# Kernel optimization log

Measured on AMD Instinct MI355X. Metric: run time of the kernel, lower is better.

Reference implementation:

```python
import jax, jax.numpy as jnp
import numpy as np

NEG = -1e30  # log-domain 'zero' (safe stand-in for -inf)


def _ctc_loss(logits, labels, label_length, logit_length):
    """Dense-label CTC loss, blank = last class, logits [B,T,C] batch-major.

    Matches tf.nn.ctc_loss(blank_index=-1, logits_time_major=False):
    per-example negative log-likelihood via the standard forward algorithm
    on the blank-extended label sequence of length S = 2L+1.
    """
    B, T, C = logits.shape
    L = labels.shape[1]
    S = 2 * L + 1
    blank = C - 1

    logp = jax.nn.log_softmax(logits, axis=-1)           # [B,T,C]
    lp_t = jnp.moveaxis(logp, 1, 0)                      # [T,B,C]

    # Extended label: blank, l1, blank, l2, ..., blank
    y_ext = jnp.full((B, S), blank, dtype=labels.dtype).at[:, 1::2].set(labels)
    s_idx = jnp.arange(S)
    # s -> s-2 skip allowed iff current symbol is a non-blank differing from s-2
    y_m2 = jnp.pad(y_ext, ((0, 0), (2, 0)), constant_values=blank)[:, :-2]
    skip = (s_idx[None, :] >= 2) & (y_ext != blank) & (y_ext != y_m2)  # [B,S]

    emit0 = jnp.take_along_axis(lp_t[0], y_ext, axis=1)  # [B,S]
    alpha0 = jnp.where(s_idx[None, :] <= 1, emit0, NEG)  # paths start at s=0 or 1

    def step(alpha, lp):
        emit = jnp.take_along_axis(lp, y_ext, axis=1)                      # [B,S]
        a1 = jnp.pad(alpha, ((0, 0), (1, 0)), constant_values=NEG)[:, :-1]  # s-1
        a2 = jnp.pad(alpha, ((0, 0), (2, 0)), constant_values=NEG)[:, :-2]  # s-2
        a2 = jnp.where(skip, a2, NEG)
        new = jnp.logaddexp(jnp.logaddexp(alpha, a1), a2) + emit
        return new, new

    _, alphas = jax.lax.scan(step, alpha0, lp_t[1:])     # [T-1,B,S]
    alphas = jnp.concatenate([alpha0[None], alphas], axis=0)  # [T,B,S]

    b = jnp.arange(B)
    final = alphas[logit_length - 1, b]                  # [B,S] alpha at last frame
    end = 2 * label_length                               # index of final blank
    nll = -jnp.logaddexp(final[b, end], final[b, end - 1])
    return jnp.mean(nll)


def setup_inputs() -> dict:
    key = jax.random.key(0)
    k1, k2, k3 = jax.random.split(key, 3)
    B, T, C, L = 256, 256, 512, 64
    logits = jax.random.normal(k1, (B, T, C), dtype=jnp.float32)
    labels = jax.random.randint(k2, (B, L), 0, C - 1, dtype=jnp.int32)  # never blank
    label_length = jax.random.randint(k3, (B,), 16, L + 1, dtype=jnp.int32)
    logit_length = jnp.full((B,), T, dtype=jnp.int32)
    return {"logits": logits, "labels": labels,
            "label_length": label_length, "logit_length": logit_length}


def reference(logits, labels, label_length, logit_length):
    return _ctc_loss(logits, labels, label_length, logit_length)
```

## Files before the change

kernel.cpp:

```cpp
#include <hip/hip_runtime.h>
#include <math.h>

#define NEGV -1e30f

constexpr int Bc = 256;
constexpr int Tc = 256;
constexpr int Cc = 512;
constexpr int Lc = 64;
constexpr int PW = 8;
constexpr int NGRP = Tc / PW;
constexpr float INVLN2 = 1.44269504088896340736f;
constexpr float LN2    = 0.69314718055994530942f;

__device__ __forceinline__ float la2(float a, float b) {
    float m = fmaxf(a, b);
    float d = fabsf(a - b);
    return m + __log2f(exp2f(-d) + 1.0f);
}

__device__ __forceinline__ float lse3(float a, float b, float c) {
    float m = fmaxf(fmaxf(a, b), c);
    return m + __log2f(exp2f(a - m) + exp2f(b - m) + exp2f(c - m));
}

__device__ __forceinline__ float dpp_shr1(float x, float fill) {
    int r = __builtin_amdgcn_update_dpp(__float_as_int(fill), __float_as_int(x),
                                        0x138 , 0xF, 0xF, false);
    return __int_as_float(r);
}

__device__ __forceinline__ float wave_sum_dpp(float v) {
#define DPPADD(ctrl)                                                          \
    v += __int_as_float(__builtin_amdgcn_update_dpp(                          \
        0, __float_as_int(v), (ctrl), 0xF, 0xF, true))
    DPPADD(0x111);
    DPPADD(0x112);
    DPPADD(0x114);
    DPPADD(0x118);
    DPPADD(0x142);
    DPPADD(0x143);
#undef DPPADD
    return __int_as_float(__builtin_amdgcn_readlane(__float_as_int(v), 63));
}

__global__ __launch_bounds__(576) void ctc_k(const float* __restrict__ logits,
                                             const int* __restrict__ labels,
                                             const int* __restrict__ lab_len,
                                             const int* __restrict__ log_len,
                                             float* __restrict__ nll) {
    const int b    = blockIdx.x;
    const int tid  = threadIdx.x;
    const int w    = tid >> 6;
    const int lane = tid & 63;

    __shared__ float em[Tc][66];
    __shared__ int   done[PW];

    if (tid < PW) done[tid] = 0;
    __syncthreads();

    const float* base = logits + (size_t)b * Tc * Cc;
    const int y = labels[b * Lc + lane];

    if (w < PW) {
        const float* a0r = base + (size_t)w * Cc;
        const float* a1r = base + (size_t)(w + PW) * Cc;
        float4 c0 = ((const float4*)a0r)[lane], c1 = ((const float4*)a0r)[lane + 64];
        float  cg = a0r[y];
        float4 d0 = ((const float4*)a1r)[lane], d1 = ((const float4*)a1r)[lane + 64];
        float  dg = a1r[y];

        for (int i = 0; i < NGRP; ++i) {
            float4 e0, e1; float eg;
            if (i + 2 < NGRP) {
                const float* ar = base + (size_t)(w + PW * (i + 2)) * Cc;
                e0 = ((const float4*)ar)[lane];
                e1 = ((const float4*)ar)[lane + 64];
                eg = ar[y];
            }
            float e = __expf(c0.x) + __expf(c0.y) + __expf(c0.z) + __expf(c0.w)
                    + __expf(c1.x) + __expf(c1.y) + __expf(c1.z) + __expf(c1.w);
            float lse2 = __log2f(wave_sum_dpp(e));
            const int t = w + PW * i;
            em[t][lane] = cg * INVLN2 - lse2;
            if (lane == 63)
                em[t][64] = c1.w * INVLN2 - lse2;
            __builtin_amdgcn_sched_barrier(0);
            asm volatile("s_waitcnt lgkmcnt(0)" ::: "memory");
            if (lane == 0) *(volatile int*)&done[w] = i + 1;
            __builtin_amdgcn_sched_barrier(0);
            c0 = d0; c1 = d1; cg = dg;
            d0 = e0; d1 = e1; dg = eg;
        }
    } else {
        const int  prevlab = __shfl_up(y, 1, 64);
        const bool skip    = (lane >= 1) && (y != prevlab);
        const int  llm1    = log_len[b] - 1;
        float ae = NEGV, ao = NEGV, ax = NEGV;
        float fe = NEGV, fo = NEGV, fx = NEGV;

        auto step = [&](float em_lv, float em_bv, int t) {
            float po = dpp_shr1(ao, NEGV);
            float nae = la2(ae, po) + em_bv;
            float nao = (skip ? lse3(ao, ae, po)
                              : la2(ao, ae)) + em_lv;
            float nax = la2(ax, ao) + em_bv;
            ae = nae; ao = nao; ax = nax;
            if (t == llm1) { fe = ae; fo = ao; fx = ax; }
        };

        for (int g = 0; g < NGRP; ++g) {
            for (;;) {
                int mn = 0x7fffffff;
#pragma unroll
                for (int pw = 0; pw < PW; ++pw)
                    mn = min(mn, *(volatile int*)&done[pw]);
                if (mn > g) break;
                __builtin_amdgcn_s_sleep(2);
            }
            asm volatile("" ::: "memory");

            float el[PW], eb[PW];
#pragma unroll
            for (int r = 0; r < PW; ++r) {
                el[r] = em[PW * g + r][lane];
                eb[r] = em[PW * g + r][64];
            }
            if (g == 0) {
                ae = (lane == 0) ? eb[0] : NEGV;
                ao = (lane == 0) ? el[0] : NEGV;
                ax = NEGV;
                if (llm1 == 0) { fe = ae; fo = ao; fx = ax; }
#pragma unroll
                for (int r = 1; r < PW; ++r) step(el[r], eb[r], r);
            } else {
#pragma unroll
                for (int r = 0; r < PW; ++r) step(el[r], eb[r], PW * g + r);
            }
        }

        const int L  = lab_len[b];
        float f0 = (L == Lc) ? __shfl(fx, 63, 64) : __shfl(fe, L, 64);
        float f1 = __shfl(fo, L - 1, 64);
        if (lane == 0) nll[b] = -LN2 * la2(f0, f1);
    }
}

__global__ __launch_bounds__(256) void reduce_k(const float* __restrict__ nll,
                                                float* __restrict__ out) {
    int tid = threadIdx.x;
    float v = nll[tid];
#pragma unroll
    for (int o = 32; o; o >>= 1) v += __shfl_xor(v, o, 64);
    __shared__ float pr[4];
    if ((tid & 63) == 0) pr[tid >> 6] = v;
    __syncthreads();
    if (tid == 0) out[0] = (pr[0] + pr[1] + pr[2] + pr[3]) * (1.0f / Bc);
}

extern "C" void kernel_launch(void* const* d_in, const int* in_sizes, int n_in,
                              void* d_out, int out_size, void* d_ws, size_t ws_size,
                              hipStream_t stream) {
    const float* logits  = (const float*)d_in[0];
    const int*   labels  = (const int*)d_in[1];
    const int*   lab_len = (const int*)d_in[2];
    const int*   log_len = (const int*)d_in[3];
    float* out = (float*)d_out;
    float* nll = (float*)d_ws;

    hipLaunchKernelGGL(ctc_k, dim3(Bc), dim3(576), 0, stream,
                       logits, labels, lab_len, log_len, nll);
    hipLaunchKernelGGL(reduce_k, dim3(1), dim3(256), 0, stream, nll, out);
}
```

Baseline: 207.0 us.

## Serialize emission and recursion phases, stage rows in LDS for label gather

Removes the dedicated recursion wave and its flag-based spin-wait handoff. All 8 waves first compute log-softmax emissions for all timesteps, with a deeper 3-row prefetch. Each row is staged in shared memory so the label gather is an LDS read rather than a scattered global load. After a block barrier, wave 0 alone runs the alpha recursion. This drops the polling and extra global gathers, but the serial recursion no longer overlaps the memory-bound emission phase, and it adds 16KB of LDS per block.

```diff
diff --git a/kernel.cpp b/kernel.cpp
--- a/kernel.cpp
+++ b/kernel.cpp
@@ -8,6 +8,7 @@
 constexpr int Cc = 512;
 constexpr int Lc = 64;
 constexpr int PW = 8;
+constexpr int NROW = Tc / PW;
 constexpr int NGRP = Tc / PW;
 constexpr float INVLN2 = 1.44269504088896340736f;
 constexpr float LN2    = 0.69314718055994530942f;
@@ -43,7 +44,7 @@
     return __int_as_float(__builtin_amdgcn_readlane(__float_as_int(v), 63));
 }
 
-__global__ __launch_bounds__(576) void ctc_k(const float* __restrict__ logits,
+__global__ __launch_bounds__(512) void ctc_k(const float* __restrict__ logits,
                                              const int* __restrict__ labels,
                                              const int* __restrict__ lab_len,
                                              const int* __restrict__ log_len,
@@ -54,96 +55,85 @@
     const int lane = tid & 63;
 
     __shared__ float em[Tc][66];
-    __shared__ int   done[PW];
-
-    if (tid < PW) done[tid] = 0;
-    __syncthreads();
+    __shared__ float rows[PW][Cc];
 
     const float* base = logits + (size_t)b * Tc * Cc;
     const int y = labels[b * Lc + lane];
 
-    if (w < PW) {
-        const float* a0r = base + (size_t)w * Cc;
-        const float* a1r = base + (size_t)(w + PW) * Cc;
-        float4 c0 = ((const float4*)a0r)[lane], c1 = ((const float4*)a0r)[lane + 64];
-        float  cg = a0r[y];
-        float4 d0 = ((const float4*)a1r)[lane], d1 = ((const float4*)a1r)[lane + 64];
-        float  dg = a1r[y];
+    {
+        float* myrow = rows[w];
+        const float4* pa = (const float4*)(base + (size_t)w * Cc);
+        const float4* pb = (const float4*)(base + (size_t)(w + PW) * Cc);
+        const float4* pc = (const float4*)(base + (size_t)(w + 2 * PW) * Cc);
+        float4 a0 = pa[lane], a1 = pa[lane + 64];
+        float4 b0 = pb[lane], b1 = pb[lane + 64];
+        float4 c0 = pc[lane], c1 = pc[lane + 64];
 
-        for (int i = 0; i < NGRP; ++i) {
-            float4 e0, e1; float eg;
-            if (i + 2 < NGRP) {
-                const float* ar = base + (size_t)(w + PW * (i + 2)) * Cc;
-                e0 = ((const float4*)ar)[lane];
-                e1 = ((const float4*)ar)[lane + 64];
-                eg = ar[y];
+        for (int i = 0; i < NROW; ++i) {
+            float4 n0, n1;
+            if (i + 3 < NROW) {
+                const float4* pn =
+                    (const float4*)(base + (size_t)(w + PW * (i + 3)) * Cc);
+                n0 = pn[lane]; n1 = pn[lane + 64];
             }
-            float e = __expf(c0.x) + __expf(c0.y) + __expf(c0.z) + __expf(c0.w)
-                    + __expf(c1.x) + __expf(c1.y) + __expf(c1.z) + __expf(c1.w);
+            float e = __expf(a0.x) + __expf(a0.y) + __expf(a0.z) + __expf(a0.w)
+                    + __expf(a1.x) + __expf(a1.y) + __expf(a1.z) + __expf(a1.w);
             float lse2 = __log2f(wave_sum_dpp(e));
+            ((float4*)myrow)[lane]      = a0;
+            ((float4*)myrow)[lane + 64] = a1;
+            float xl = myrow[y];
             const int t = w + PW * i;
-            em[t][lane] = cg * INVLN2 - lse2;
+            em[t][lane] = xl * INVLN2 - lse2;
             if (lane == 63)
-                em[t][64] = c1.w * INVLN2 - lse2;
-            __builtin_amdgcn_sched_barrier(0);
-            asm volatile("s_waitcnt lgkmcnt(0)" ::: "memory");
-            if (lane == 0) *(volatile int*)&done[w] = i + 1;
-            __builtin_amdgcn_sched_barrier(0);
-            c0 = d0; c1 = d1; cg = dg;
-            d0 = e0; d1 = e1; dg = eg;
+                em[t][64] = a1.w * INVLN2 - lse2;
+            a0 = b0; a1 = b1;
+            b0 = c0; b1 = c1;
+            c0 = n0; c1 = n1;
         }
-    } else {
-        const int  prevlab = __shfl_up(y, 1, 64);
-        const bool skip    = (lane >= 1) && (y != prevlab);
-        const int  llm1    = log_len[b] - 1;
-        float ae = NEGV, ao = NEGV, ax = NEGV;
-        float fe = NEGV, fo = NEGV, fx = NEGV;
+    }
+    __syncthreads();
+    if (w != 0) return;
 
-        auto step = [&](float em_lv, float em_bv, int t) {
-            float po = dpp_shr1(ao, NEGV);
-            float nae = la2(ae, po) + em_bv;
-            float nao = (skip ? lse3(ao, ae, po)
-                              : la2(ao, ae)) + em_lv;
-            float nax = la2(ax, ao) + em_bv;
-            ae = nae; ao = nao; ax = nax;
-            if (t == llm1) { fe = ae; fo = ao; fx = ax; }
-        };
+    const int  prevlab = __shfl_up(y, 1, 64);
+    const bool skip    = (lane >= 1) && (y != prevlab);
+    const int  llm1    = log_len[b] - 1;
+    float ae = NEGV, ao = NEGV, ax = NEGV;
+    float fe = NEGV, fo = NEGV, fx = NEGV;
 
-        for (int g = 0; g < NGRP; ++g) {
-            for (;;) {
-                int mn = 0x7fffffff;
+    auto step = [&](float em_lv, float em_bv, int t) {
+        float po = dpp_shr1(ao, NEGV);
+        float nae = la2(ae, po) + em_bv;
+        float nao = (skip ? lse3(ao, ae, po)
+                          : la2(ao, ae)) + em_lv;
+        float nax = la2(ax, ao) + em_bv;
+        ae = nae; ao = nao; ax = nax;
+        if (t == llm1) { fe = ae; fo = ao; fx = ax; }
+    };
+
+    for (int g = 0; g < NGRP; ++g) {
+        float el[PW], eb[PW];
 #pragma unroll
-                for (int pw = 0; pw < PW; ++pw)
-                    mn = min(mn, *(volatile int*)&done[pw]);
-                if (mn > g) break;
-                __builtin_amdgcn_s_sleep(2);
-            }
-            asm volatile("" ::: "memory");
+        for (int r = 0; r < PW; ++r) {
+            el[r] = em[PW * g + r][lane];
+            eb[r] = em[PW * g + r][64];
+        }
+        if (g == 0) {
+            ae = (lane == 0) ? eb[0] : NEGV;
+            ao = (lane == 0) ? el[0] : NEGV;
+            ax = NEGV;
+            if (llm1 == 0) { fe = ae; fo = ao; fx = ax; }
+#pragma unroll
+            for (int r = 1; r < PW; ++r) step(el[r], eb[r], r);
+        } else {
+#pragma unroll
+            for (int r = 0; r < PW; ++r) step(el[r], eb[r], PW * g + r);
+        }
+    }
 
-            float el[PW], eb[PW];
-#pragma unroll
-            for (int r = 0; r < PW; ++r) {
-                el[r] = em[PW * g + r][lane];
-                eb[r] = em[PW * g + r][64];
-            }
-            if (g == 0) {
-                ae = (lane == 0) ? eb[0] : NEGV;
-                ao = (lane == 0) ? el[0] : NEGV;
-                ax = NEGV;
-                if (llm1 == 0) { fe = ae; fo = ao; fx = ax; }
-#pragma unroll
-                for (int r = 1; r < PW; ++r) step(el[r], eb[r], r);
-            } else {
-#pragma unroll
-                for (int r = 0; r < PW; ++r) step(el[r], eb[r], PW * g + r);
-            }
-        }
-
-        const int L  = lab_len[b];
-        float f0 = (L == Lc) ? __shfl(fx, 63, 64) : __shfl(fe, L, 64);
-        float f1 = __shfl(fo, L - 1, 64);
-        if (lane == 0) nll[b] = -LN2 * la2(f0, f1);
-    }
+    const int L  = lab_len[b];
+    float f0 = (L == Lc) ? __shfl(fx, 63, 64) : __shfl(fe, L, 64);
+    float f1 = __shfl(fo, L - 1, 64);
+    if (lane == 0) nll[b] = -LN2 * la2(f0, f1);
 }
 
 __global__ __launch_bounds__(256) void reduce_k(const float* __restrict__ nll,
@@ -168,7 +158,7 @@
     float* out = (float*)d_out;
     float* nll = (float*)d_ws;
 
-    hipLaunchKernelGGL(ctc_k, dim3(Bc), dim3(576), 0, stream,
+    hipLaunchKernelGGL(ctc_k, dim3(Bc), dim3(512), 0, stream,
                        logits, labels, lab_len, log_len, nll);
     hipLaunchKernelGGL(reduce_k, dim3(1), dim3(256), 0, stream, nll, out);
 }
```

Measured after the change: 239.9 us. 15.9% more time.
